# Performance work log

Hardware: AMD Instinct MI355X
Metric: run time of the kernel (lower is better)

Reference implementation:

```python
import jax, jax.numpy as jnp
import numpy as np

B, C, H, W = 2, 128, 96, 96
HEADS, DHEAD, WIN = 4, 32, 5
INNER = HEADS * DHEAD
PAD = WIN // 2


def setup_inputs() -> dict:
    key = jax.random.key(0)
    k1, k2, k3, k4, k5 = jax.random.split(key, 5)
    s = 1.0 / np.sqrt(C)
    return {
        "x": jax.random.normal(k1, (B, C, H, W), dtype=jnp.float32),
        "wq": jax.random.normal(k2, (INNER, C), dtype=jnp.float32) * s,
        "wk": jax.random.normal(k3, (INNER, C), dtype=jnp.float32) * s,
        "wv": jax.random.normal(k4, (INNER, C), dtype=jnp.float32) * s,
        "wproj": jax.random.normal(k5, (C, INNER), dtype=jnp.float32) * s,
    }


def _windows(t):
    # same neighborhood ordering as F.unfold (row-major over kernel offsets).
    tp = jnp.pad(t, ((0, 0), (0, 0), (0, 0), (PAD, PAD), (PAD, PAD)))
    wins = [tp[:, :, :, di:di + H, dj:dj + W]
            for di in range(WIN) for dj in range(WIN)]
    return jnp.stack(wins, axis=3)


def reference(x, wq, wk, wv, wproj):
    # 1x1 convs == per-pixel linear maps
    q = jnp.einsum('oc,bcxy->boxy', wq, x).reshape(B, HEADS, DHEAD, H, W)
    k = jnp.einsum('oc,bcxy->boxy', wk, x).reshape(B, HEADS, DHEAD, H, W)
    v = jnp.einsum('oc,bcxy->boxy', wv, x).reshape(B, HEADS, DHEAD, H, W)

    k_win = _windows(k)  # (B,h,d,25,H,W)
    v_win = _windows(v)

    scale = 1.0 / np.sqrt(DHEAD)
    attn = jnp.einsum('bhdxy,bhdkxy->bhkxy', q, k_win) * scale
    attn = jax.nn.softmax(attn, axis=2)  # softmax over the 25 window positions
    out = jnp.einsum('bhkxy,bhdkxy->bhdxy', attn, v_win)

    out = out.reshape(B, INNER, H, W)
    return jnp.einsum('co,boxy->bcxy', wproj, out)
```

## Files before the change

kernel.cpp:

```cpp
#include <hip/hip_runtime.h>
#include <hip/hip_fp16.h>

#define PP 9216

typedef _Float16 f16x8 __attribute__((ext_vector_type(8)));
typedef _Float16 f16x4 __attribute__((ext_vector_type(4)));
typedef float    f32x4 __attribute__((ext_vector_type(4)));

#define SXW 136
#define SVW 72
#define SSW 68

#define OFF_X   0
#define OFF_K   17408
#define OFF_VT  34816
#define OFF_Q   53248
#define OFF_P   57600
#define OFF_AO  66816
#define OFF_INV 71168
#define LDS_BYTES 71424

__device__ __forceinline__ f16x8 cvt8(float4 u0, float4 u1) {
    f16x8 r;
    r[0] = (_Float16)u0.x; r[1] = (_Float16)u0.y;
    r[2] = (_Float16)u0.z; r[3] = (_Float16)u0.w;
    r[4] = (_Float16)u1.x; r[5] = (_Float16)u1.y;
    r[6] = (_Float16)u1.z; r[7] = (_Float16)u1.w;
    return r;
}

__global__ __launch_bounds__(256, 2) void fused_attn(
    const float* __restrict__ x,  const float* __restrict__ wq,
    const float* __restrict__ wk, const float* __restrict__ wv,
    const float* __restrict__ wp, float* __restrict__ out)
{
    __shared__ __align__(16) char smem[LDS_BYTES];
    _Float16* sX  = (_Float16*)(smem + OFF_X);
    float*    sS  = (float*)   (smem + OFF_X);
    _Float16* sK  = (_Float16*)(smem + OFF_K);
    _Float16* sVT = (_Float16*)(smem + OFF_VT);
    _Float16* sQ  = (_Float16*)(smem + OFF_Q);
    _Float16* sP  = (_Float16*)(smem + OFF_P);
    _Float16* sAo = (_Float16*)(smem + OFF_AO);
    float*    sInv= (float*)   (smem + OFF_INV);

    const int t = threadIdx.x;
    const int w = t >> 6, lane = t & 63, lm = lane & 15, quad = lane >> 4;
    const int x0 = blockIdx.x * 4, y0 = blockIdx.y * 4, b = blockIdx.z;
    const float* xb = x + (size_t)b * 128 * PP;
    float* ob = out + (size_t)b * 128 * PP;

    #pragma unroll
    for (int i = 0; i < 16; i++) {
        int c   = i * 8 + (t >> 5);
        int pos = (t & 31) * 2;
        int gy = y0 - 2 + (pos >> 3);
        int gx = x0 - 2 + (pos & 7);
        float2 v = make_float2(0.f, 0.f);
        if ((unsigned)gy < 96u && (unsigned)gx < 96u)
            v = *(const float2*)(xb + (size_t)c * PP + gy * 96 + gx);
        sX[pos * SXW + c]       = (_Float16)v.x;
        sX[(pos + 1) * SXW + c] = (_Float16)v.y;
    }

    f16x8 BKV[4][4];
    #pragma unroll
    for (int ni = 0; ni < 4; ni++) {
        int n = w + 4 * ni;
        const float* wr = (ni < 2) ? (wk + (size_t)(n * 16 + lm) * 128)
                                   : (wv + (size_t)((n - 8) * 16 + lm) * 128);
        #pragma unroll
        for (int kc = 0; kc < 4; kc++)
            BKV[ni][kc] = cvt8(*(const float4*)(wr + kc * 32 + quad * 8),
                               *(const float4*)(wr + kc * 32 + quad * 8 + 4));
    }
    f16x8 BQ[2][4];
    #pragma unroll
    for (int nn = 0; nn < 2; nn++) {
        const float* wr = wq + (size_t)((w * 2 + nn) * 16 + lm) * 128;
        #pragma unroll
        for (int kc = 0; kc < 4; kc++)
            BQ[nn][kc] = cvt8(*(const float4*)(wr + kc * 32 + quad * 8),
                              *(const float4*)(wr + kc * 32 + quad * 8 + 4));
    }
    __syncthreads();

    #pragma unroll
    for (int m = 0; m < 4; m++) {
        f16x8 A[4];
        #pragma unroll
        for (int kc = 0; kc < 4; kc++)
            A[kc] = *(const f16x8*)(sX + (m * 16 + lm) * SXW + kc * 32 + quad * 8);
        #pragma unroll
        for (int ni = 0; ni < 4; ni++) {
            f32x4 acc = {0.f, 0.f, 0.f, 0.f};
            #pragma unroll
            for (int kc = 0; kc < 4; kc++)
                acc = __builtin_amdgcn_mfma_f32_16x16x32_f16(A[kc], BKV[ni][kc], acc, 0, 0, 0);
            int n = w + 4 * ni;
            if (ni < 2) {
                #pragma unroll
                for (int r = 0; r < 4; r++)
                    sK[(m * 16 + quad * 4 + r) * SXW + n * 16 + lm] = (_Float16)acc[r];
            } else {
                f16x4 tv;
                #pragma unroll
                for (int r = 0; r < 4; r++) tv[r] = (_Float16)acc[r];
                *(f16x4*)(sVT + ((n - 8) * 16 + lm) * SVW + m * 16 + quad * 4) = tv;
            }
        }
    }

    {
        int hrow = ((lm >> 2) + 2) * 8 + (lm & 3) + 2;
        f16x8 A[4];
        #pragma unroll
        for (int kc = 0; kc < 4; kc++)
            A[kc] = *(const f16x8*)(sX + hrow * SXW + kc * 32 + quad * 8);
        #pragma unroll
        for (int nn = 0; nn < 2; nn++) {
            f32x4 acc = {0.f, 0.f, 0.f, 0.f};
            #pragma unroll
            for (int kc = 0; kc < 4; kc++)
                acc = __builtin_amdgcn_mfma_f32_16x16x32_f16(A[kc], BQ[nn][kc], acc, 0, 0, 0);
            int n = w * 2 + nn;
            #pragma unroll
            for (int r = 0; r < 4; r++)
                sQ[(quad * 4 + r) * SXW + n * 16 + lm] = (_Float16)acc[r];
        }
    }
    __syncthreads();

    {
        const int h = w;
        float*    sSh = sS + h * 16 * SSW;
        _Float16* sPh = sP + h * 16 * SVW;

        f16x8 Aq = *(const f16x8*)(sQ + lm * SXW + h * 32 + quad * 8);
        #pragma unroll
        for (int n = 0; n < 4; n++) {
            f16x8 Bk = *(const f16x8*)(sK + (n * 16 + lm) * SXW + h * 32 + quad * 8);
            f32x4 acc = {0.f, 0.f, 0.f, 0.f};
            acc = __builtin_amdgcn_mfma_f32_16x16x32_f16(Aq, Bk, acc, 0, 0, 0);
            #pragma unroll
            for (int r = 0; r < 4; r++)
                sSh[(quad * 4 + r) * SSW + n * 16 + lm] = acc[r];
        }

        const int spx = lane >> 2, sub = lane & 3;
        const int py = spx >> 2, pxx = spx & 3;
        float sv[16];
        #pragma unroll
        for (int j4 = 0; j4 < 4; j4++)
            *(float4*)(sv + j4 * 4) = *(const float4*)(sSh + spx * SSW + sub * 16 + j4 * 4);
        const float scale = 0.17677669529663689f;
        float sj[16];
        float mx = -1e30f;
        #pragma unroll
        for (int j = 0; j < 16; j++) {
            int pos = sub * 16 + j;
            int hy = pos >> 3, hx = pos & 7;
            bool memb = (hy >= py) & (hy < py + 5) & (hx >= pxx) & (hx < pxx + 5);
            sj[j] = memb ? sv[j] * scale : -1e30f;
            mx = fmaxf(mx, sj[j]);
        }
        mx = fmaxf(mx, __shfl_xor(mx, 1));
        mx = fmaxf(mx, __shfl_xor(mx, 2));
        float sum = 0.f;
        f16x8 ev[2];
        #pragma unroll
        for (int j = 0; j < 16; j++) {
            float e = __expf(sj[j] - mx);
            sum += e;
            ev[j >> 3][j & 7] = (_Float16)e;
        }
        sum += __shfl_xor(sum, 1);
        sum += __shfl_xor(sum, 2);
        *(f16x8*)(sPh + spx * SVW + sub * 16)     = ev[0];
        *(f16x8*)(sPh + spx * SVW + sub * 16 + 8) = ev[1];
        if (sub == 0) sInv[h * 16 + spx] = 1.f / sum;

        f16x8 Ap[2];
        #pragma unroll
        for (int kk = 0; kk < 2; kk++)
            Ap[kk] = *(const f16x8*)(sPh + lm * SVW + kk * 32 + quad * 8);
        float ivr[4];
        *(float4*)ivr = *(const float4*)(sInv + h * 16 + quad * 4);
        #pragma unroll
        for (int n = 0; n < 2; n++) {
            f32x4 acc = {0.f, 0.f, 0.f, 0.f};
            #pragma unroll
            for (int kk = 0; kk < 2; kk++) {
                f16x8 Bv = *(const f16x8*)(sVT + (h * 32 + n * 16 + lm) * SVW + kk * 32 + quad * 8);
                acc = __builtin_amdgcn_mfma_f32_16x16x32_f16(Ap[kk], Bv, acc, 0, 0, 0);
            }
            #pragma unroll
            for (int r = 0; r < 4; r++)
                sAo[(quad * 4 + r) * SXW + h * 32 + n * 16 + lm] =
                    (_Float16)(acc[r] * ivr[r]);
        }
    }
    __syncthreads();

    {
        f16x8 Aw[2][4];
        #pragma unroll
        for (int mi = 0; mi < 2; mi++) {
            const float* wr = wp + (size_t)((w * 2 + mi) * 16 + lm) * 128;
            #pragma unroll
            for (int kc = 0; kc < 4; kc++)
                Aw[mi][kc] = cvt8(*(const float4*)(wr + kc * 32 + quad * 8),
                                  *(const float4*)(wr + kc * 32 + quad * 8 + 4));
        }
        f16x8 Bf[4];
        #pragma unroll
        for (int kc = 0; kc < 4; kc++)
            Bf[kc] = *(const f16x8*)(sAo + lm * SXW + kc * 32 + quad * 8);
        int gp = (y0 + (lm >> 2)) * 96 + x0 + (lm & 3);
        #pragma unroll
        for (int mi = 0; mi < 2; mi++) {
            f32x4 acc = {0.f, 0.f, 0.f, 0.f};
            #pragma unroll
            for (int kc = 0; kc < 4; kc++)
                acc = __builtin_amdgcn_mfma_f32_16x16x32_f16(Aw[mi][kc], Bf[kc], acc, 0, 0, 0);
            int c0 = (w * 2 + mi) * 16 + quad * 4;
            #pragma unroll
            for (int r = 0; r < 4; r++)
                ob[(size_t)(c0 + r) * PP + gp] = acc[r];
        }
    }
}

extern "C" void kernel_launch(void* const* d_in, const int* in_sizes, int n_in,
                              void* d_out, int out_size, void* d_ws, size_t ws_size,
                              hipStream_t stream)
{
    const float* x  = (const float*)d_in[0];
    const float* wq = (const float*)d_in[1];
    const float* wk = (const float*)d_in[2];
    const float* wv = (const float*)d_in[3];
    const float* wp = (const float*)d_in[4];
    float* out = (float*)d_out;

    fused_attn<<<dim3(24, 24, 2), 256, 0, stream>>>(x, wq, wk, wv, wp, out);
}
```

Before: 123.4 us.

## Pre-convert weights to fp16, shrink LDS footprint, raise occupancy, remap blocks

```diff
diff --git a/kernel.cpp b/kernel.cpp
--- a/kernel.cpp
+++ b/kernel.cpp
@@ -5,48 +5,66 @@
 
 typedef _Float16 f16x8 __attribute__((ext_vector_type(8)));
 typedef _Float16 f16x4 __attribute__((ext_vector_type(4)));
+typedef _Float16 h2    __attribute__((ext_vector_type(2)));
 typedef float    f32x4 __attribute__((ext_vector_type(4)));
 
 #define SXW 136
+#define SSW 68
+#define SPW 72
 #define SVW 72
-#define SSW 68
-
-#define OFF_X   0
-#define OFF_K   17408
-#define OFF_VT  34816
-#define OFF_Q   53248
-#define OFF_P   57600
-#define OFF_AO  66816
-#define OFF_INV 71168
-#define LDS_BYTES 71424
-
-__device__ __forceinline__ f16x8 cvt8(float4 u0, float4 u1) {
-    f16x8 r;
-    r[0] = (_Float16)u0.x; r[1] = (_Float16)u0.y;
-    r[2] = (_Float16)u0.z; r[3] = (_Float16)u0.w;
-    r[4] = (_Float16)u1.x; r[5] = (_Float16)u1.y;
-    r[6] = (_Float16)u1.z; r[7] = (_Float16)u1.w;
-    return r;
+
+#define OFF_X    0
+#define OFF_K    17408
+#define OFF_Q    35840
+#define OFF_INV  40192
+#define LDS_BYTES 40448
+
+__global__ __launch_bounds__(256) void prep_w(
+    const float* __restrict__ wq, const float* __restrict__ wk,
+    const float* __restrict__ wv, const float* __restrict__ wp,
+    _Float16* __restrict__ wqkv16, _Float16* __restrict__ wp16)
+{
+    int e = (blockIdx.x * 256 + threadIdx.x) * 4;
+    const float* src;
+    _Float16* dst;
+    if (e < 49152) {
+        int o = e >> 7;
+        src = (o < 128) ? (wq + (size_t)o * 128)
+            : (o < 256) ? (wk + (size_t)(o - 128) * 128)
+                        : (wv + (size_t)(o - 256) * 128);
+        src += (e & 127);
+        dst = wqkv16 + e;
+    } else {
+        int j = e - 49152;
+        src = wp + j;
+        dst = wp16 + j;
+    }
+    float4 v = *(const float4*)src;
+    f16x4 h;
+    h[0] = (_Float16)v.x; h[1] = (_Float16)v.y;
+    h[2] = (_Float16)v.z; h[3] = (_Float16)v.w;
+    *(f16x4*)dst = h;
 }
 
-__global__ __launch_bounds__(256, 2) void fused_attn(
-    const float* __restrict__ x,  const float* __restrict__ wq,
-    const float* __restrict__ wk, const float* __restrict__ wv,
-    const float* __restrict__ wp, float* __restrict__ out)
+__global__ __launch_bounds__(256, 4) void fused_attn(
+    const float* __restrict__ x, const _Float16* __restrict__ wqkv,
+    const _Float16* __restrict__ wp16, float* __restrict__ out)
 {
     __shared__ __align__(16) char smem[LDS_BYTES];
     _Float16* sX  = (_Float16*)(smem + OFF_X);
-    float*    sS  = (float*)   (smem + OFF_X);
     _Float16* sK  = (_Float16*)(smem + OFF_K);
-    _Float16* sVT = (_Float16*)(smem + OFF_VT);
     _Float16* sQ  = (_Float16*)(smem + OFF_Q);
-    _Float16* sP  = (_Float16*)(smem + OFF_P);
-    _Float16* sAo = (_Float16*)(smem + OFF_AO);
-    float*    sInv= (float*)   (smem + OFF_INV);
+    _Float16* sAo = (_Float16*)(smem + OFF_Q);
+    float*    sInv= (float*)(smem + OFF_INV);
 
     const int t = threadIdx.x;
     const int w = t >> 6, lane = t & 63, lm = lane & 15, quad = lane >> 4;
-    const int x0 = blockIdx.x * 4, y0 = blockIdx.y * 4, b = blockIdx.z;
+
+    const int wgid = (blockIdx.x & 7) * 144 + (blockIdx.x >> 3);
+    const int b = wgid / 576;
+    const int rem = wgid - b * 576;
+    const int x0 = (rem % 24) * 4, y0 = (rem / 24) * 4;
+
     const float* xb = x + (size_t)b * 128 * PP;
     float* ob = out + (size_t)b * 128 * PP;
 
@@ -62,29 +80,9 @@
         sX[pos * SXW + c]       = (_Float16)v.x;
         sX[(pos + 1) * SXW + c] = (_Float16)v.y;
     }
-
-    f16x8 BKV[4][4];
-    #pragma unroll
-    for (int ni = 0; ni < 4; ni++) {
-        int n = w + 4 * ni;
-        const float* wr = (ni < 2) ? (wk + (size_t)(n * 16 + lm) * 128)
-                                   : (wv + (size_t)((n - 8) * 16 + lm) * 128);
-        #pragma unroll
-        for (int kc = 0; kc < 4; kc++)
-            BKV[ni][kc] = cvt8(*(const float4*)(wr + kc * 32 + quad * 8),
-                               *(const float4*)(wr + kc * 32 + quad * 8 + 4));
-    }
-    f16x8 BQ[2][4];
-    #pragma unroll
-    for (int nn = 0; nn < 2; nn++) {
-        const float* wr = wq + (size_t)((w * 2 + nn) * 16 + lm) * 128;
-        #pragma unroll
-        for (int kc = 0; kc < 4; kc++)
-            BQ[nn][kc] = cvt8(*(const float4*)(wr + kc * 32 + quad * 8),
-                              *(const float4*)(wr + kc * 32 + quad * 8 + 4));
-    }
-    __syncthreads();
-
+    __syncthreads();
+
+    h2 vpk[2][4][2];
     #pragma unroll
     for (int m = 0; m < 4; m++) {
         f16x8 A[4];
@@ -92,22 +90,28 @@
         for (int kc = 0; kc < 4; kc++)
             A[kc] = *(const f16x8*)(sX + (m * 16 + lm) * SXW + kc * 32 + quad * 8);
         #pragma unroll
-        for (int ni = 0; ni < 4; ni++) {
-            f32x4 acc = {0.f, 0.f, 0.f, 0.f};
-            #pragma unroll
-            for (int kc = 0; kc < 4; kc++)
-                acc = __builtin_amdgcn_mfma_f32_16x16x32_f16(A[kc], BKV[ni][kc], acc, 0, 0, 0);
+        for (int ni = 0; ni < 2; ni++) {
             int n = w + 4 * ni;
-            if (ni < 2) {
-                #pragma unroll
-                for (int r = 0; r < 4; r++)
-                    sK[(m * 16 + quad * 4 + r) * SXW + n * 16 + lm] = (_Float16)acc[r];
-            } else {
-                f16x4 tv;
-                #pragma unroll
-                for (int r = 0; r < 4; r++) tv[r] = (_Float16)acc[r];
-                *(f16x4*)(sVT + ((n - 8) * 16 + lm) * SVW + m * 16 + quad * 4) = tv;
-            }
+            const _Float16* wr = wqkv + (size_t)(128 + n * 16 + lm) * 128;
+            f32x4 acc = {0.f, 0.f, 0.f, 0.f};
+            #pragma unroll
+            for (int kc = 0; kc < 4; kc++)
+                acc = __builtin_amdgcn_mfma_f32_16x16x32_f16(
+                    A[kc], *(const f16x8*)(wr + kc * 32 + quad * 8), acc, 0, 0, 0);
+            #pragma unroll
+            for (int r = 0; r < 4; r++)
+                sK[(m * 16 + quad * 4 + r) * SXW + n * 16 + lm] = (_Float16)acc[r];
+        }
+        #pragma unroll
+        for (int nn = 0; nn < 2; nn++) {
+            const _Float16* wr = wqkv + (size_t)(256 + (2 * w + nn) * 16 + lm) * 128;
+            f32x4 acc = {0.f, 0.f, 0.f, 0.f};
+            #pragma unroll
+            for (int kc = 0; kc < 4; kc++)
+                acc = __builtin_amdgcn_mfma_f32_16x16x32_f16(
+                    A[kc], *(const f16x8*)(wr + kc * 32 + quad * 8), acc, 0, 0, 0);
+            vpk[nn][m][0][0] = (_Float16)acc[0]; vpk[nn][m][0][1] = (_Float16)acc[1];
+            vpk[nn][m][1][0] = (_Float16)acc[2]; vpk[nn][m][1][1] = (_Float16)acc[3];
         }
     }
 
@@ -119,34 +123,36 @@
             A[kc] = *(const f16x8*)(sX + hrow * SXW + kc * 32 + quad * 8);
         #pragma unroll
         for (int nn = 0; nn < 2; nn++) {
-            f32x4 acc = {0.f, 0.f, 0.f, 0.f};
-            #pragma unroll
-            for (int kc = 0; kc < 4; kc++)
-                acc = __builtin_amdgcn_mfma_f32_16x16x32_f16(A[kc], BQ[nn][kc], acc, 0, 0, 0);
-            int n = w * 2 + nn;
-            #pragma unroll
-            for (int r = 0; r < 4; r++)
-                sQ[(quad * 4 + r) * SXW + n * 16 + lm] = (_Float16)acc[r];
-        }
-    }
-    __syncthreads();
-
-    {
-        const int h = w;
-        float*    sSh = sS + h * 16 * SSW;
-        _Float16* sPh = sP + h * 16 * SVW;
-
-        f16x8 Aq = *(const f16x8*)(sQ + lm * SXW + h * 32 + quad * 8);
+            const _Float16* wr = wqkv + (size_t)((2 * w + nn) * 16 + lm) * 128;
+            f32x4 acc = {0.f, 0.f, 0.f, 0.f};
+            #pragma unroll
+            for (int kc = 0; kc < 4; kc++)
+                acc = __builtin_amdgcn_mfma_f32_16x16x32_f16(
+                    A[kc], *(const f16x8*)(wr + kc * 32 + quad * 8), acc, 0, 0, 0);
+            #pragma unroll
+            for (int r = 0; r < 4; r++)
+                sQ[(quad * 4 + r) * SXW + (2 * w + nn) * 16 + lm] = (_Float16)acc[r];
+        }
+    }
+    __syncthreads();
+
+    float*    sSh = (float*)(smem + OFF_X + w * 4352);
+    _Float16* sPh = (_Float16*)(smem + OFF_X + w * 4352);
+
+    {
+        f16x8 Aq = *(const f16x8*)(sQ + lm * SXW + w * 32 + quad * 8);
         #pragma unroll
         for (int n = 0; n < 4; n++) {
-            f16x8 Bk = *(const f16x8*)(sK + (n * 16 + lm) * SXW + h * 32 + quad * 8);
+            f16x8 Bk = *(const f16x8*)(sK + (n * 16 + lm) * SXW + w * 32 + quad * 8);
             f32x4 acc = {0.f, 0.f, 0.f, 0.f};
             acc = __builtin_amdgcn_mfma_f32_16x16x32_f16(Aq, Bk, acc, 0, 0, 0);
             #pragma unroll
             for (int r = 0; r < 4; r++)
                 sSh[(quad * 4 + r) * SSW + n * 16 + lm] = acc[r];
         }
-
+    }
+
+    {
         const int spx = lane >> 2, sub = lane & 3;
         const int py = spx >> 2, pxx = spx & 3;
         float sv[16];
@@ -167,51 +173,55 @@
         mx = fmaxf(mx, __shfl_xor(mx, 1));
         mx = fmaxf(mx, __shfl_xor(mx, 2));
         float sum = 0.f;
-        f16x8 ev[2];
+        f16x8 ev0, ev1;
         #pragma unroll
         for (int j = 0; j < 16; j++) {
             float e = __expf(sj[j] - mx);
             sum += e;
-            ev[j >> 3][j & 7] = (_Float16)e;
+            if (j < 8) ev0[j] = (_Float16)e; else ev1[j - 8] = (_Float16)e;
         }
         sum += __shfl_xor(sum, 1);
         sum += __shfl_xor(sum, 2);
-        *(f16x8*)(sPh + spx * SVW + sub * 16)     = ev[0];
-        *(f16x8*)(sPh + spx * SVW + sub * 16 + 8) = ev[1];
-        if (sub == 0) sInv[h * 16 + spx] = 1.f / sum;
-
+        *(f16x8*)(sPh + spx * SPW + sub * 16)     = ev0;
+        *(f16x8*)(sPh + spx * SPW + sub * 16 + 8) = ev1;
+        if (sub == 0) sInv[w * 16 + spx] = 1.f / sum;
+    }
+    __syncthreads();
+
+    _Float16* sVh = (_Float16*)(smem + OFF_K + w * 4608);
+    #pragma unroll
+    for (int nn = 0; nn < 2; nn++)
+        #pragma unroll
+        for (int m = 0; m < 4; m++)
+            #pragma unroll
+            for (int rp = 0; rp < 2; rp++)
+                *(h2*)(sVh + (nn * 16 + lm) * SVW + m * 16 + quad * 4 + rp * 2)
+                    = vpk[nn][m][rp];
+
+    {
         f16x8 Ap[2];
         #pragma unroll
-        for (int kk = 0; kk < 2; kk++)
-            Ap[kk] = *(const f16x8*)(sPh + lm * SVW + kk * 32 + quad * 8);
+        for (int kc = 0; kc < 2; kc++)
+            Ap[kc] = *(const f16x8*)(sPh + lm * SPW + kc * 32 + quad * 8);
         float ivr[4];
-        *(float4*)ivr = *(const float4*)(sInv + h * 16 + quad * 4);
-        #pragma unroll
-        for (int n = 0; n < 2; n++) {
-            f32x4 acc = {0.f, 0.f, 0.f, 0.f};
-            #pragma unroll
-            for (int kk = 0; kk < 2; kk++) {
-                f16x8 Bv = *(const f16x8*)(sVT + (h * 32 + n * 16 + lm) * SVW + kk * 32 + quad * 8);
-                acc = __builtin_amdgcn_mfma_f32_16x16x32_f16(Ap[kk], Bv, acc, 0, 0, 0);
+        *(float4*)ivr = *(const float4*)(sInv + w * 16 + quad * 4);
+        #pragma unroll
+        for (int nd = 0; nd < 2; nd++) {
+            f32x4 acc = {0.f, 0.f, 0.f, 0.f};
+            #pragma unroll
+            for (int kc = 0; kc < 2; kc++) {
+                f16x8 Bv = *(const f16x8*)(sVh + (nd * 16 + lm) * SVW + kc * 32 + quad * 8);
+                acc = __builtin_amdgcn_mfma_f32_16x16x32_f16(Ap[kc], Bv, acc, 0, 0, 0);
             }
             #pragma unroll
             for (int r = 0; r < 4; r++)
-                sAo[(quad * 4 + r) * SXW + h * 32 + n * 16 + lm] =
+                sAo[(quad * 4 + r) * SXW + w * 32 + nd * 16 + lm] =
                     (_Float16)(acc[r] * ivr[r]);
         }
     }
     __syncthreads();
 
     {
-        f16x8 Aw[2][4];
-        #pragma unroll
-        for (int mi = 0; mi < 2; mi++) {
-            const float* wr = wp + (size_t)((w * 2 + mi) * 16 + lm) * 128;
-            #pragma unroll
-            for (int kc = 0; kc < 4; kc++)
-                Aw[mi][kc] = cvt8(*(const float4*)(wr + kc * 32 + quad * 8),
-                                  *(const float4*)(wr + kc * 32 + quad * 8 + 4));
-        }
         f16x8 Bf[4];
         #pragma unroll
         for (int kc = 0; kc < 4; kc++)
@@ -219,10 +229,12 @@
         int gp = (y0 + (lm >> 2)) * 96 + x0 + (lm & 3);
         #pragma unroll
         for (int mi = 0; mi < 2; mi++) {
-            f32x4 acc = {0.f, 0.f, 0.f, 0.f};
-            #pragma unroll
-            for (int kc = 0; kc < 4; kc++)
-                acc = __builtin_amdgcn_mfma_f32_16x16x32_f16(Aw[mi][kc], Bf[kc], acc, 0, 0, 0);
+            const _Float16* wr = wp16 + (size_t)((w * 2 + mi) * 16 + lm) * 128;
+            f32x4 acc = {0.f, 0.f, 0.f, 0.f};
+            #pragma unroll
+            for (int kc = 0; kc < 4; kc++)
+                acc = __builtin_amdgcn_mfma_f32_16x16x32_f16(
+                    *(const f16x8*)(wr + kc * 32 + quad * 8), Bf[kc], acc, 0, 0, 0);
             int c0 = (w * 2 + mi) * 16 + quad * 4;
             #pragma unroll
             for (int r = 0; r < 4; r++)
@@ -242,5 +254,9 @@
     const float* wp = (const float*)d_in[4];
     float* out = (float*)d_out;
 
-    fused_attn<<<dim3(24, 24, 2), 256, 0, stream>>>(x, wq, wk, wv, wp, out);
+    _Float16* wqkv16 = (_Float16*)d_ws;
+    _Float16* wp16   = wqkv16 + 49152;
+
+    prep_w<<<dim3(64), 256, 0, stream>>>(wq, wk, wv, wp, wqkv16, wp16);
+    fused_attn<<<dim3(1152), 256, 0, stream>>>(x, wqkv16, wp16, out);
 }
```

Result: faster. 107.9 us (-12.6%).
